# Performance work log

Measured on AMD Instinct MI355X. Metric: run time of the kernel, lower is better.

Reference implementation:

```python
import jax, jax.numpy as jnp
import numpy as np

D_MODEL = 1024
N_HEADS = 16
D_HEAD = D_MODEL // N_HEADS
D_FF = 4096
MAX_ITERS = 2
B, T = 8, 1024
LN_EPS = 1e-5


def _layernorm(x, g, b):
    m = jnp.mean(x, axis=-1, keepdims=True)
    v = jnp.mean(jnp.square(x - m), axis=-1, keepdims=True)
    return (x - m) * jax.lax.rsqrt(v + LN_EPS) * g + b


def setup_inputs() -> dict:
    key = jax.random.key(0)
    ks = jax.random.split(key, 16)
    s = 0.02
    inp = {
        "z": jax.random.normal(ks[0], (B, T, D_MODEL), dtype=jnp.float32),
        # per-head Q/K/V projections stacked over heads: [H, D, Dh], bias [H, Dh]
        "Wq": jax.random.normal(ks[1], (N_HEADS, D_MODEL, D_HEAD), dtype=jnp.float32) * s,
        "bq": jnp.zeros((N_HEADS, D_HEAD), dtype=jnp.float32),
        "Wk": jax.random.normal(ks[2], (N_HEADS, D_MODEL, D_HEAD), dtype=jnp.float32) * s,
        "bk": jnp.zeros((N_HEADS, D_HEAD), dtype=jnp.float32),
        "Wv": jax.random.normal(ks[3], (N_HEADS, D_MODEL, D_HEAD), dtype=jnp.float32) * s,
        "bv": jnp.zeros((N_HEADS, D_HEAD), dtype=jnp.float32),
        "Wo": jax.random.normal(ks[4], (D_MODEL, D_MODEL), dtype=jnp.float32) * s,
        "bo": jnp.zeros((D_MODEL,), dtype=jnp.float32),
        "W1": jax.random.normal(ks[5], (D_MODEL, D_FF), dtype=jnp.float32) * s,
        "b1": jnp.zeros((D_FF,), dtype=jnp.float32),
        "W2": jax.random.normal(ks[6], (D_FF, D_MODEL), dtype=jnp.float32) * s,
        "b2": jnp.zeros((D_MODEL,), dtype=jnp.float32),
        "g1": jnp.ones((D_MODEL,), dtype=jnp.float32),
        "be1": jnp.zeros((D_MODEL,), dtype=jnp.float32),
        "g2": jnp.ones((D_MODEL,), dtype=jnp.float32),
        "be2": jnp.zeros((D_MODEL,), dtype=jnp.float32),
    }
    return inp


def reference(z, Wq, bq, Wk, bk, Wv, bv, Wo, bo, W1, b1, W2, b2, g1, be1, g2, be2):
    # Controller outputs (alphas/state/aux) are unused by the original forward -> omitted.
    # Dropout is inference-identity.
    scale = 1.0 / jnp.sqrt(jnp.asarray(D_HEAD, dtype=z.dtype))
    z_refined = z
    for _ in range(MAX_ITERS):
        # batched per-head projections: [B,H,T,Dh]
        q = jnp.einsum('btd,hdk->bhtk', z, Wq) + bq[None, :, None, :]
        k = jnp.einsum('btd,hdk->bhtk', z, Wk) + bk[None, :, None, :]
        v = jnp.einsum('btd,hdk->bhtk', z, Wv) + bv[None, :, None, :]
        scores = jnp.einsum('bhtk,bhsk->bhts', q, k) * scale  # [B,H,T,T]
        attn = jax.nn.softmax(scores, axis=-1)
        o = jnp.einsum('bhts,bhsk->bhtk', attn, v)  # [B,H,T,Dh]
        # concat heads in order (matches torch.cat over head list)
        o = jnp.transpose(o, (0, 2, 1, 3)).reshape(z.shape[0], z.shape[1], D_MODEL)
        attn_out = o @ Wo + bo
        z = _layernorm(z + attn_out, g1, be1)
        z_refined = z
        ffn = jnp.maximum(z @ W1 + b1, 0.0) @ W2 + b2
        z = _layernorm(z + ffn, g2, be2)
    return z_refined
```

## Files before the change

kernel.cpp:

```cpp
#include <hip/hip_runtime.h>
#include <hip/hip_bf16.h>

typedef __bf16 bf16t;
typedef bf16t bf16x4 __attribute__((ext_vector_type(4)));
typedef bf16t bf16x8 __attribute__((ext_vector_type(8)));
typedef float f32x4 __attribute__((ext_vector_type(4)));

#define BT 8192
#define TT 1024
#define DM 1024
#define DFF 4096
#define QSCALE 0.18033688011112042f

static __device__ __forceinline__ f32x4 mfma16(bf16x8 a, bf16x8 b, f32x4 c) {
  return __builtin_amdgcn_mfma_f32_16x16x32_bf16(a, b, c, 0, 0, 0);
}
static __device__ __forceinline__ f32x4 f4zero() {
  f32x4 z = {0.f, 0.f, 0.f, 0.f};
  return z;
}
static __device__ __forceinline__ f32x4 vmax4(f32x4 a, f32x4 b) {
  f32x4 r;
#pragma unroll
  for (int i = 0; i < 4; i++) r[i] = fmaxf(a[i], b[i]);
  return r;
}
static __device__ __forceinline__ void gld16(const bf16t* g, bf16t* l) {
  __builtin_amdgcn_global_load_lds((const __attribute__((address_space(1))) void*)g,
                                   (__attribute__((address_space(3))) void*)l, 16, 0, 0);
}
static __device__ __forceinline__ int cperm(int c) {
  return (c & ~31) + (((c >> 2) & 3) << 3) + (((c >> 4) & 1) << 2) + (c & 3);
}

__global__ __launch_bounds__(256) void cvtz_kernel(const float* __restrict__ in,
                                                   bf16t* __restrict__ outp,
                                                   bf16t* __restrict__ outn, long n) {
  long i = ((long)blockIdx.x * 256 + threadIdx.x) * 4;
  if (i >= n) return;
  f32x4 v = *(const f32x4*)&in[i];
  bf16x4 o = {(bf16t)v[0], (bf16t)v[1], (bf16t)v[2], (bf16t)v[3]};
  *(bf16x4*)&outn[i] = o;
  int lo = (int)(i & 1023);
  long p = (i - lo) + cperm(lo);
  *(bf16x4*)&outp[p] = o;
}

__global__ __launch_bounds__(256) void tcvt_kernel(const float* __restrict__ in,
                                                   bf16t* __restrict__ out, int M, int N) {
  __shared__ float T[64][65];
  const int t = threadIdx.x;
  const int ty = t >> 6, tx = t & 63;
  const long n0 = (long)blockIdx.x * 64, m0 = (long)blockIdx.y * 64;
#pragma unroll
  for (int p = 0; p < 16; ++p) {
    int a = ty * 16 + p;
    T[a][tx] = in[(m0 + a) * N + n0 + tx];
  }
  __syncthreads();
#pragma unroll
  for (int p = 0; p < 16; ++p) {
    int r = ty * 16 + p;
    out[(n0 + r) * M + m0 + cperm(tx)] = (bf16t)T[tx][r];
  }
}

__global__ __launch_bounds__(256) void vtrans_kernel(const bf16t* __restrict__ qkv,
                                                     bf16t* __restrict__ vT) {
  __shared__ bf16t T[64][72];
  const int bh = blockIdx.x;
  const int b = bh >> 4, h = bh & 15;
  const int tt = blockIdx.y;
  const int t = threadIdx.x;
  const int ty = t >> 6, tx = t & 63;
  const long srcbase = ((long)b * TT + tt * 64) * 3072 + 2048 + h * 64;
#pragma unroll
  for (int p = 0; p < 16; ++p) {
    int a = ty * 16 + p;
    T[a][tx] = qkv[srcbase + (long)a * 3072 + tx];
  }
  __syncthreads();
  const long dstbase = ((long)bh * 64) * 1024 + tt * 64;
  const int txp = cperm(tx);
#pragma unroll
  for (int p = 0; p < 16; ++p) {
    int d = ty * 16 + p;
    vT[dstbase + (long)d * 1024 + txp] = T[tx][d];
  }
}

__global__ __launch_bounds__(256) void pack_qkv_t_kernel(const float* __restrict__ Wq,
                                                         const float* __restrict__ Wk,
                                                         const float* __restrict__ Wv,
                                                         bf16t* __restrict__ WT) {
  __shared__ float T[64][65];
  const int bx = blockIdx.x;
  const int sel = bx >> 4, h = bx & 15;
  const float* src = ((sel == 0) ? Wq : (sel == 1) ? Wk : Wv) + (long)h * 65536;
  const long nbase = (long)sel * 1024 + h * 64;
  const long m0 = (long)blockIdx.y * 64;
  const int t = threadIdx.x;
  const int ty = t >> 6, tx = t & 63;
#pragma unroll
  for (int p = 0; p < 16; ++p) {
    int a = ty * 16 + p;
    T[a][tx] = src[(m0 + a) * 64 + tx];
  }
  __syncthreads();
#pragma unroll
  for (int p = 0; p < 16; ++p) {
    int r = ty * 16 + p;
    WT[(nbase + r) * 1024 + m0 + cperm(tx)] = (bf16t)T[tx][r];
  }
}

__global__ __launch_bounds__(256) void pack_bias_kernel(const float* __restrict__ bq,
                                                        const float* __restrict__ bk,
                                                        const float* __restrict__ bv,
                                                        float* __restrict__ bqkv) {
  int i = blockIdx.x * 256 + threadIdx.x;
  if (i >= 3072) return;
  int sel = i >> 10, c = i & 1023;
  bqkv[i] = ((sel == 0) ? bq : (sel == 1) ? bk : bv)[c];
}

template <int EPI>
__global__ __launch_bounds__(256) void gemm_kernel(
    const bf16t* __restrict__ A, const bf16t* __restrict__ Bt,
    const float* __restrict__ bias, const bf16t* __restrict__ resid,
    void* __restrict__ Cout, int M, int N, int K) {
  __shared__ __align__(16) bf16t As[3 * 128 * 32];
  __shared__ __align__(16) bf16t Bs[3 * 128 * 32];
  const int tid = threadIdx.x;
  const int lane = tid & 63;
  const int wid = tid >> 6;
  const int wr = wid >> 1, wc = wid & 1;
  const int g = lane >> 4, lr = lane & 15;

  const int gy = M >> 7;
  const int nwg = gridDim.x;
  const int chunk = nwg >> 3;
  const int wg = blockIdx.x;
  const int lid = (wg & 7) * chunk + (wg >> 3);
  const int gsz = gy << 3;
  const int group = lid / gsz;
  const int rem = lid - group * gsz;
  const int rr = rem >> 3;
  const int cc = (group << 3) + (rem & 7);
  const long brow = (long)rr * 128;
  const long bcol = (long)cc * 128;

  f32x4 acc[4][4];
#pragma unroll
  for (int i = 0; i < 4; i++)
#pragma unroll
    for (int j = 0; j < 4; j++) acc[i][j] = f4zero();

  const int srow = tid >> 2;
  const int csrc = (tid & 3) ^ ((tid >> 3) & 3);
  const bf16t* gA = &A[(brow + srow) * (long)K + 8 * csrc];
  const bf16t* gB = &Bt[(bcol + srow) * (long)K + 8 * csrc];
  bf16t* lA = As + wid * 512;
  bf16t* lB = Bs + wid * 512;

  auto stage = [&](int buf, int k0) {
    gld16(gA + k0, lA + buf * 4096);
    gld16(gA + k0 + (long)64 * K, lA + buf * 4096 + 2048);
    gld16(gB + k0, lB + buf * 4096);
    gld16(gB + k0 + (long)64 * K, lB + buf * 4096 + 2048);
  };
  auto ldf = [&](const bf16t* buf, int row) -> bf16x8 {
    return *(const bf16x8*)(buf + row * 32 + ((((row >> 1) ^ g) & 3) << 3));
  };

  const int nt = K >> 5;
  stage(0, 0);
  stage(1, 32);
  asm volatile("s_waitcnt vmcnt(4)" ::: "memory");
  __builtin_amdgcn_s_barrier();
  __builtin_amdgcn_sched_barrier(0);

  for (int t = 0; t < nt; ++t) {
    const int k2 = (t + 2) << 5;
    const bool pf = (k2 < K);
    if (pf) stage((t + 2) % 3, k2);

    const bf16t* bufA = As + (t % 3) * 4096;
    const bf16t* bufB = Bs + (t % 3) * 4096;
    bf16x8 af[4], bfv[4];
#pragma unroll
    for (int i = 0; i < 4; i++) af[i] = ldf(bufA, wr * 64 + i * 16 + lr);
#pragma unroll
    for (int j = 0; j < 4; j++) bfv[j] = ldf(bufB, wc * 64 + j * 16 + lr);
#pragma unroll
    for (int i = 0; i < 4; i++)
#pragma unroll
      for (int j = 0; j < 4; j++) acc[i][j] = mfma16(af[i], bfv[j], acc[i][j]);

    if (t + 1 < nt) {
      if (pf)
        asm volatile("s_waitcnt vmcnt(4)" ::: "memory");
      else
        asm volatile("s_waitcnt vmcnt(0)" ::: "memory");
      __builtin_amdgcn_s_barrier();
      __builtin_amdgcn_sched_barrier(0);
    }
  }

#pragma unroll
  for (int j = 0; j < 4; j++) {
    int col = (int)bcol + wc * 64 + j * 16 + lr;
    float bval = bias ? bias[col] : 0.f;
#pragma unroll
    for (int i = 0; i < 4; i++) {
      long row0 = brow + wr * 64 + i * 16 + 4 * g;
#pragma unroll
      for (int r2 = 0; r2 < 4; r2++) {
        long row = row0 + r2;
        float v = acc[i][j][r2] + bval;
        if (EPI == 0) {
          float vv = (col < 1024) ? v * QSCALE : v;
          int oc = (col < 2048) ? cperm(col) : col;
          ((bf16t*)Cout)[row * N + oc] = (bf16t)vv;
        } else if (EPI == 1) {
          ((bf16t*)Cout)[row * N + cperm(col)] = (bf16t)fmaxf(v, 0.f);
        } else {
          ((bf16t*)Cout)[row * N + col] = (bf16t)(v + (float)resid[row * N + col]);
        }
      }
    }
  }
}

__global__ __launch_bounds__(256) void attn_kernel(const bf16t* __restrict__ qkv,
                                                   const bf16t* __restrict__ vT,
                                                   bf16t* __restrict__ o) {
  const int bh = blockIdx.x;
  const int b = bh >> 4, h = bh & 15;
  const int qt = blockIdx.y;
  const int tid = threadIdx.x;
  const int lane = tid & 63;
  const int w = tid >> 6;
  const int g = lane >> 4, lr = lane & 15;

  __shared__ __align__(16) bf16t Qs[2 * 64 * 32];
  __shared__ __align__(16) bf16t Ks[2][2 * 64 * 32];
  __shared__ __align__(16) bf16t Vs[2][2 * 64 * 32];

  const long rowbase = (long)b * TT;
  const long qrow0 = rowbase + (long)qt * 64;

  const int sq = tid >> 2;
  const int sco = (((tid & 3) ^ ((tid >> 3) & 3))) * 8;

  const bf16t* qsrc = &qkv[(qrow0 + sq) * 3072 + h * 64 + sco];
  const bf16t* ksrc = &qkv[(rowbase + sq) * 3072 + 1024 + h * 64 + sco];
  const bf16t* vsrc = &vT[((long)bh * 64 + sq) * 1024 + sco];
  const int wbase = w * 512;

  auto stageQ = [&]() {
    gld16(qsrc, Qs + wbase);
    gld16(qsrc + 32, Qs + 2048 + wbase);
  };
  auto stageK = [&](int buf, int kt) {
    const bf16t* s = ksrc + (long)kt * 64 * 3072;
    gld16(s, Ks[buf] + wbase);
    gld16(s + 32, Ks[buf] + 2048 + wbase);
  };
  auto stageV = [&](int buf, int kt) {
    const bf16t* s = vsrc + kt * 64;
    gld16(s, Vs[buf] + wbase);
    gld16(s + 32, Vs[buf] + 2048 + wbase);
  };
  auto ldf = [&](const bf16t* base, int hh, int row) -> bf16x8 {
    return *(const bf16x8*)(base + hh * 2048 + row * 32 + ((((row >> 1) ^ g) & 3) << 3));
  };

  stageQ();
  stageK(0, 0);
  stageV(0, 0);
  __syncthreads();

  const int qr = w * 16 + lr;
  const bf16x8 qb_lo = ldf(Qs, 0, qr);
  const bf16x8 qb_hi = ldf(Qs, 1, qr);

  f32x4 acc_o[4];
#pragma unroll
  for (int j = 0; j < 4; j++) acc_o[j] = f4zero();
  float mrun = -1e30f, lrun = 0.f;

  int cur = 0;
  for (int kt = 0; kt < 16; ++kt) {
    if (kt < 15) {
      stageK(cur ^ 1, kt + 1);
      stageV(cur ^ 1, kt + 1);
    }

    f32x4 s[4];
#pragma unroll
    for (int jt = 0; jt < 4; jt++) {
      int krow = jt * 16 + lr;
      bf16x8 ka_lo = ldf(Ks[cur], 0, krow);
      bf16x8 ka_hi = ldf(Ks[cur], 1, krow);
      f32x4 t = f4zero();
      t = mfma16(ka_lo, qb_lo, t);
      t = mfma16(ka_hi, qb_hi, t);
      s[jt] = t;
    }

    f32x4 mv = vmax4(vmax4(s[0], s[1]), vmax4(s[2], s[3]));
    float tm = fmaxf(fmaxf(mv[0], mv[1]), fmaxf(mv[2], mv[3]));
    tm = fmaxf(tm, __shfl_xor(tm, 16, 64));
    tm = fmaxf(tm, __shfl_xor(tm, 32, 64));

    if (__any(tm > mrun + 11.5f)) {
      float mnew = fmaxf(mrun, tm);
      float corr = __builtin_amdgcn_exp2f(mrun - mnew);
      mrun = mnew;
      lrun *= corr;
#pragma unroll
      for (int r = 0; r < 4; r++) {
        float cq = __shfl(corr, 20 * g + r, 64);
#pragma unroll
        for (int dt = 0; dt < 4; dt++) acc_o[dt][r] *= cq;
      }
    }

    f32x4 sv = f4zero();
#pragma unroll
    for (int jt = 0; jt < 4; jt++)
#pragma unroll
      for (int r = 0; r < 4; r++) {
        float pv = __builtin_amdgcn_exp2f(s[jt][r] - mrun);
        s[jt][r] = pv;
        sv[r] += pv;
      }
    float tsum = sv[0] + sv[1] + sv[2] + sv[3];
    tsum += __shfl_xor(tsum, 16, 64);
    tsum += __shfl_xor(tsum, 32, 64);
    lrun += tsum;

    bf16x8 pa0, pa1;
#pragma unroll
    for (int r = 0; r < 4; r++) {
      pa0[r] = (bf16t)s[0][r];
      pa0[r + 4] = (bf16t)s[1][r];
      pa1[r] = (bf16t)s[2][r];
      pa1[r + 4] = (bf16t)s[3][r];
    }

#pragma unroll
    for (int dt = 0; dt < 4; dt++) {
      int vrow = dt * 16 + lr;
      bf16x8 vb_lo = ldf(Vs[cur], 0, vrow);
      bf16x8 vb_hi = ldf(Vs[cur], 1, vrow);
      acc_o[dt] = mfma16(pa0, vb_lo, acc_o[dt]);
      acc_o[dt] = mfma16(pa1, vb_hi, acc_o[dt]);
    }

    __syncthreads();
    cur ^= 1;
  }

  float inv = 1.0f / lrun;
#pragma unroll
  for (int r = 0; r < 4; r++) {
    float iq = __shfl(inv, 20 * g + r, 64);
    long row = qrow0 + w * 16 + 4 * g + r;
#pragma unroll
    for (int dt = 0; dt < 4; dt++) {
      o[row * (long)DM + cperm(h * 64 + dt * 16 + lr)] = (bf16t)(acc_o[dt][r] * iq);
    }
  }
}

__global__ __launch_bounds__(256) void ln_kernel(const bf16t* __restrict__ x,
                                                 const float* __restrict__ gamma,
                                                 const float* __restrict__ beta,
                                                 bf16t* __restrict__ out_act,
                                                 bf16t* __restrict__ out_res,
                                                 float* __restrict__ out_f32) {
  const long row = blockIdx.x;
  const int tid = threadIdx.x;
  const int idx = tid * 4;
  bf16x4 xv = *(const bf16x4*)&x[row * DM + idx];
  float v[4];
#pragma unroll
  for (int c = 0; c < 4; c++) v[c] = (float)xv[c];
  float s = v[0] + v[1] + v[2] + v[3];
  float ss = v[0] * v[0] + v[1] * v[1] + v[2] * v[2] + v[3] * v[3];
#pragma unroll
  for (int m = 1; m < 64; m <<= 1) {
    s += __shfl_xor(s, m, 64);
    ss += __shfl_xor(ss, m, 64);
  }
  __shared__ float red[8];
  const int w = tid >> 6, lane = tid & 63;
  if (lane == 0) {
    red[w] = s;
    red[4 + w] = ss;
  }
  __syncthreads();
  s = red[0] + red[1] + red[2] + red[3];
  ss = red[4] + red[5] + red[6] + red[7];
  float mean = s * (1.f / DM);
  float var = ss * (1.f / DM) - mean * mean;
  float inv = rsqrtf(var + 1e-5f);
  f32x4 ga = *(const f32x4*)&gamma[idx];
  f32x4 be = *(const f32x4*)&beta[idx];
  float y[4];
#pragma unroll
  for (int c = 0; c < 4; c++) y[c] = (v[c] - mean) * inv * ga[c] + be[c];
  if (out_act) {
    bf16x4 ob = {(bf16t)y[0], (bf16t)y[1], (bf16t)y[2], (bf16t)y[3]};
    *(bf16x4*)&out_act[row * DM + cperm(idx)] = ob;
  }
  if (out_res) {
    bf16x4 ob = {(bf16t)y[0], (bf16t)y[1], (bf16t)y[2], (bf16t)y[3]};
    *(bf16x4*)&out_res[row * DM + idx] = ob;
  }
  if (out_f32) {
    f32x4 of = {y[0], y[1], y[2], y[3]};
    *(f32x4*)&out_f32[row * DM + idx] = of;
  }
}

extern "C" void kernel_launch(void* const* d_in, const int* in_sizes, int n_in,
                              void* d_out, int out_size, void* d_ws, size_t ws_size,
                              hipStream_t stream) {
  const float* z = (const float*)d_in[0];
  const float* Wq = (const float*)d_in[1];
  const float* bq = (const float*)d_in[2];
  const float* Wk = (const float*)d_in[3];
  const float* bk = (const float*)d_in[4];
  const float* Wv = (const float*)d_in[5];
  const float* bv = (const float*)d_in[6];
  const float* Wo = (const float*)d_in[7];
  const float* bo = (const float*)d_in[8];
  const float* W1 = (const float*)d_in[9];
  const float* b1 = (const float*)d_in[10];
  const float* W2 = (const float*)d_in[11];
  const float* b2 = (const float*)d_in[12];
  const float* g1 = (const float*)d_in[13];
  const float* be1 = (const float*)d_in[14];
  const float* g2 = (const float*)d_in[15];
  const float* be2 = (const float*)d_in[16];

  char* p = (char*)d_ws;
  auto alloc = [&](size_t bytes) {
    char* r = p;
    p += (bytes + 255) & ~(size_t)255;
    return r;
  };
  bf16t* wqkvT = (bf16t*)alloc((size_t)3072 * 1024 * 2);
  float* bqkv = (float*)alloc((size_t)3072 * 4);
  bf16t* woT = (bf16t*)alloc((size_t)1024 * 1024 * 2);
  bf16t* w1T = (bf16t*)alloc((size_t)4096 * 1024 * 2);
  bf16t* w2T = (bf16t*)alloc((size_t)1024 * 4096 * 2);
  bf16t* act = (bf16t*)alloc((size_t)BT * 1024 * 2);
  bf16t* zbf = (bf16t*)alloc((size_t)BT * 1024 * 2);
  bf16t* obuf = (bf16t*)alloc((size_t)BT * 1024 * 2);
  bf16t* big = (bf16t*)alloc((size_t)BT * 4096 * 2);
  bf16t* tbuf = (bf16t*)alloc((size_t)BT * 1024 * 2);
  bf16t* residf = (bf16t*)alloc((size_t)BT * 1024 * 2);
  bf16t* vT = (bf16t*)tbuf;

  pack_qkv_t_kernel<<<dim3(48, 16), dim3(256), 0, stream>>>(Wq, Wk, Wv, wqkvT);
  pack_bias_kernel<<<dim3(12), dim3(256), 0, stream>>>(bq, bk, bv, bqkv);
  tcvt_kernel<<<dim3(16, 16), dim3(256), 0, stream>>>(Wo, woT, 1024, 1024);
  tcvt_kernel<<<dim3(64, 16), dim3(256), 0, stream>>>(W1, w1T, 1024, 4096);
  tcvt_kernel<<<dim3(16, 64), dim3(256), 0, stream>>>(W2, w2T, 4096, 1024);
  cvtz_kernel<<<dim3(8192), dim3(256), 0, stream>>>(z, act, zbf, (long)BT * 1024);

  for (int iter = 0; iter < 2; ++iter) {
    gemm_kernel<0><<<dim3(1536), dim3(256), 0, stream>>>(
        act, wqkvT, bqkv, (const bf16t*)nullptr, (void*)big, BT, 3072, 1024);
    vtrans_kernel<<<dim3(128, 16), dim3(256), 0, stream>>>(big, vT);
    attn_kernel<<<dim3(128, 16), dim3(256), 0, stream>>>(big, vT, obuf);
    const bf16t* rsrc = (iter == 0) ? zbf : residf;
    gemm_kernel<2><<<dim3(512), dim3(256), 0, stream>>>(
        obuf, woT, bo, rsrc, (void*)tbuf, BT, 1024, 1024);
    if (iter == 1) {
      ln_kernel<<<dim3(8192), dim3(256), 0, stream>>>(tbuf, g1, be1, (bf16t*)nullptr,
                                                      (bf16t*)nullptr, (float*)d_out);
      break;
    }
    ln_kernel<<<dim3(8192), dim3(256), 0, stream>>>(tbuf, g1, be1, act, residf,
                                                    (float*)nullptr);
    gemm_kernel<1><<<dim3(2048), dim3(256), 0, stream>>>(
        act, w1T, b1, (const bf16t*)nullptr, (void*)big, BT, 4096, 1024);
    gemm_kernel<2><<<dim3(512), dim3(256), 0, stream>>>(
        big, w2T, b2, residf, (void*)tbuf, BT, 1024, 4096);
    ln_kernel<<<dim3(8192), dim3(256), 0, stream>>>(tbuf, g2, be2, act, residf,
                                                    (float*)nullptr);
  }
}
```

Baseline: 574.3 us.

## Add 256x128-tile GEMM for QKV/FFN1 and fuse V transpose into epilogue

Adds a new GEMM kernel with 256x128 output tiles, double-buffered LDS and launch_bounds(256,2), used for the QKV projection and the first FFN matmul. Its QKV epilogue writes the V columns directly in transposed per-head layout, so the separate vtrans kernel and its extra pass over V in memory are removed. The larger tile raises data reuse per block but doubles accumulator registers and drops from three-stage to two-stage buffering with a full barrier every k-step, which can reduce latency hiding.

```diff
diff --git a/kernel.cpp b/kernel.cpp
--- a/kernel.cpp
+++ b/kernel.cpp
@@ -62,30 +62,6 @@
   for (int p = 0; p < 16; ++p) {
     int r = ty * 16 + p;
     out[(n0 + r) * M + m0 + cperm(tx)] = (bf16t)T[tx][r];
-  }
-}
-
-__global__ __launch_bounds__(256) void vtrans_kernel(const bf16t* __restrict__ qkv,
-                                                     bf16t* __restrict__ vT) {
-  __shared__ bf16t T[64][72];
-  const int bh = blockIdx.x;
-  const int b = bh >> 4, h = bh & 15;
-  const int tt = blockIdx.y;
-  const int t = threadIdx.x;
-  const int ty = t >> 6, tx = t & 63;
-  const long srcbase = ((long)b * TT + tt * 64) * 3072 + 2048 + h * 64;
-#pragma unroll
-  for (int p = 0; p < 16; ++p) {
-    int a = ty * 16 + p;
-    T[a][tx] = qkv[srcbase + (long)a * 3072 + tx];
-  }
-  __syncthreads();
-  const long dstbase = ((long)bh * 64) * 1024 + tt * 64;
-  const int txp = cperm(tx);
-#pragma unroll
-  for (int p = 0; p < 16; ++p) {
-    int d = ty * 16 + p;
-    vT[dstbase + (long)d * 1024 + txp] = T[tx][d];
   }
 }
 
@@ -125,6 +101,115 @@
 }
 
 template <int EPI>
+__global__ __launch_bounds__(256, 2) void gemmBig_kernel(
+    const bf16t* __restrict__ A, const bf16t* __restrict__ Bt,
+    const float* __restrict__ bias, bf16t* __restrict__ Cout,
+    bf16t* __restrict__ vTout, int M, int N, int K) {
+  __shared__ __align__(16) bf16t As[2 * 256 * 32];
+  __shared__ __align__(16) bf16t Bs[2 * 128 * 32];
+  const int tid = threadIdx.x;
+  const int lane = tid & 63;
+  const int wid = tid >> 6;
+  const int wm = wid >> 1;
+  const int wn = wid & 1;
+  const int g = lane >> 4, lr = lane & 15;
+
+  const int gy = M >> 8;
+  const int nwg = gridDim.x;
+  const int chunk = nwg >> 3;
+  const int wg = blockIdx.x;
+  const int lid = (wg & 7) * chunk + (wg >> 3);
+  const int gsz = gy << 3;
+  const int group = lid / gsz;
+  const int rem = lid - group * gsz;
+  const int rr = rem >> 3;
+  const int cc = (group << 3) + (rem & 7);
+  const long brow = (long)rr * 256;
+  const long bcol = (long)cc * 128;
+
+  f32x4 acc[8][4];
+#pragma unroll
+  for (int i = 0; i < 8; i++)
+#pragma unroll
+    for (int j = 0; j < 4; j++) acc[i][j] = f4zero();
+
+  const int srow = tid >> 2;
+  const int csrc = (tid & 3) ^ ((tid >> 3) & 3);
+  const bf16t* gA = &A[(brow + srow) * (long)K + 8 * csrc];
+  const bf16t* gB = &Bt[(bcol + srow) * (long)K + 8 * csrc];
+  bf16t* lA = As + wid * 512;
+  bf16t* lB = Bs + wid * 512;
+
+  auto stage = [&](int buf, int k0) {
+#pragma unroll
+    for (int c = 0; c < 4; ++c)
+      gld16(gA + k0 + (long)(c * 64) * K, lA + buf * 8192 + c * 2048);
+#pragma unroll
+    for (int c = 0; c < 2; ++c)
+      gld16(gB + k0 + (long)(c * 64) * K, lB + buf * 4096 + c * 2048);
+  };
+  auto ldfA = [&](int buf, int row) -> bf16x8 {
+    return *(const bf16x8*)(As + buf * 8192 + row * 32 + ((((row >> 1) ^ g) & 3) << 3));
+  };
+  auto ldfB = [&](int buf, int row) -> bf16x8 {
+    return *(const bf16x8*)(Bs + buf * 4096 + row * 32 + ((((row >> 1) ^ g) & 3) << 3));
+  };
+
+  const int nt = K >> 5;
+  stage(0, 0);
+  __syncthreads();
+
+  for (int t = 0; t < nt; ++t) {
+    const int buf = t & 1;
+    if (t + 1 < nt) stage(buf ^ 1, (t + 1) << 5);
+
+    bf16x8 a[8], b[4];
+#pragma unroll
+    for (int i = 0; i < 8; i++) a[i] = ldfA(buf, wm * 128 + i * 16 + lr);
+#pragma unroll
+    for (int j = 0; j < 4; j++) b[j] = ldfB(buf, wn * 64 + j * 16 + lr);
+#pragma unroll
+    for (int i = 0; i < 8; i++)
+#pragma unroll
+      for (int j = 0; j < 4; j++) acc[i][j] = mfma16(a[i], b[j], acc[i][j]);
+
+    __syncthreads();
+  }
+
+#pragma unroll
+  for (int j = 0; j < 4; j++) {
+    int col = (int)bcol + wn * 64 + j * 16 + lr;
+    float bval = bias ? bias[col] : 0.f;
+#pragma unroll
+    for (int i = 0; i < 8; i++) {
+      long row0 = brow + wm * 128 + i * 16 + 4 * g;
+      if (EPI == 0 && col >= 2048) {
+        int h2 = (col - 2048) >> 6, d = col & 63;
+        long bb = row0 >> 10;
+        int t0 = (int)(row0 & 1023);
+        long idx = ((((bb << 4) + h2) << 6) + d) * 1024 + cperm(t0);
+        bf16x4 ov;
+#pragma unroll
+        for (int r2 = 0; r2 < 4; r2++) ov[r2] = (bf16t)(acc[i][j][r2] + bval);
+        *(bf16x4*)&vTout[idx] = ov;
+      } else {
+#pragma unroll
+        for (int r2 = 0; r2 < 4; r2++) {
+          long row = row0 + r2;
+          float v = acc[i][j][r2] + bval;
+          if (EPI == 0) {
+            float vv = (col < 1024) ? v * QSCALE : v;
+            Cout[row * N + cperm(col)] = (bf16t)vv;
+          } else {
+            Cout[row * N + cperm(col)] = (bf16t)fmaxf(v, 0.f);
+          }
+        }
+      }
+    }
+  }
+}
+
+template <int EPI>
 __global__ __launch_bounds__(256) void gemm_kernel(
     const bf16t* __restrict__ A, const bf16t* __restrict__ Bt,
     const float* __restrict__ bias, const bf16t* __restrict__ resid,
@@ -218,15 +303,7 @@
       for (int r2 = 0; r2 < 4; r2++) {
         long row = row0 + r2;
         float v = acc[i][j][r2] + bval;
-        if (EPI == 0) {
-          float vv = (col < 1024) ? v * QSCALE : v;
-          int oc = (col < 2048) ? cperm(col) : col;
-          ((bf16t*)Cout)[row * N + oc] = (bf16t)vv;
-        } else if (EPI == 1) {
-          ((bf16t*)Cout)[row * N + cperm(col)] = (bf16t)fmaxf(v, 0.f);
-        } else {
-          ((bf16t*)Cout)[row * N + col] = (bf16t)(v + (float)resid[row * N + col]);
-        }
+        ((bf16t*)Cout)[row * N + col] = (bf16t)(v + (float)resid[row * N + col]);
       }
     }
   }
@@ -474,9 +551,8 @@
   cvtz_kernel<<<dim3(8192), dim3(256), 0, stream>>>(z, act, zbf, (long)BT * 1024);
 
   for (int iter = 0; iter < 2; ++iter) {
-    gemm_kernel<0><<<dim3(1536), dim3(256), 0, stream>>>(
-        act, wqkvT, bqkv, (const bf16t*)nullptr, (void*)big, BT, 3072, 1024);
-    vtrans_kernel<<<dim3(128, 16), dim3(256), 0, stream>>>(big, vT);
+    gemmBig_kernel<0><<<dim3(768), dim3(256), 0, stream>>>(
+        act, wqkvT, bqkv, big, vT, BT, 3072, 1024);
     attn_kernel<<<dim3(128, 16), dim3(256), 0, stream>>>(big, vT, obuf);
     const bf16t* rsrc = (iter == 0) ? zbf : residf;
     gemm_kernel<2><<<dim3(512), dim3(256), 0, stream>>>(
@@ -488,8 +564,8 @@
     }
     ln_kernel<<<dim3(8192), dim3(256), 0, stream>>>(tbuf, g1, be1, act, residf,
                                                     (float*)nullptr);
-    gemm_kernel<1><<<dim3(2048), dim3(256), 0, stream>>>(
-        act, w1T, b1, (const bf16t*)nullptr, (void*)big, BT, 4096, 1024);
+    gemmBig_kernel<1><<<dim3(1024), dim3(256), 0, stream>>>(
+        act, w1T, b1, big, (bf16t*)nullptr, BT, 4096, 1024);
     gemm_kernel<2><<<dim3(512), dim3(256), 0, stream>>>(
         big, w2T, b2, residf, (void*)tbuf, BT, 1024, 4096);
     ln_kernel<<<dim3(8192), dim3(256), 0, stream>>>(tbuf, g2, be2, act, residf,
```

Result: no change. 583.6 us (+1.6%).
